# Performance work log

Hardware: AMD Instinct MI355X
Metric: run time of the kernel (lower is better)

## Reference

```python
import jax, jax.numpy as jnp
import numpy as np

N = 8192
EPS = 1e-6


def setup_inputs() -> dict:
    key = jax.random.key(0)
    k1, k2, k3, k4 = jax.random.split(key, 4)
    P_risk = jax.random.normal(k1, (N,), dtype=jnp.float32)
    P_surv = jax.random.normal(k2, (N,), dtype=jnp.float32)
    T = jax.random.uniform(k3, (N,), dtype=jnp.float32)
    E = jax.random.randint(k4, (N,), 0, 2, dtype=jnp.int32)
    return {"P_risk": P_risk, "P_surv": P_surv, "T": T, "E": E}


def _compute_loss(P, M, E_eff):
    # P: [N] log-hazards, M: [N, N] float mask, E_eff: [N] effective event weights
    P_exp = jnp.exp(P)
    # sum_j M[i, j] * exp(P[j])  -- masked risk-set sum as a matvec
    P_exp_sum = M @ P_exp
    log_ratio = jnp.log(P_exp / (P_exp_sum + EPS))
    return -jnp.sum(log_ratio * E_eff) / jnp.sum(E_eff)


def reference(P_risk, P_surv, T, E):
    Ef = E.astype(jnp.float32)
    # M_risk[i, j] = 1 if T[i] < T[j]
    M_risk = (T[:, None] < T[None, :]).astype(jnp.float32)
    # M_surv[i, j] = 1 if T[i] > T[j] and E[j] == 1
    M_surv = (T[:, None] > T[None, :]).astype(jnp.float32) * Ef[None, :]

    # mode='risk': E * (row of M_risk nonempty)
    E_risk = Ef * (jnp.sum(M_risk, axis=1) > 0).astype(jnp.float32)
    # mode='surv': just (row of M_surv nonempty)
    E_surv = (jnp.sum(M_surv, axis=1) > 0).astype(jnp.float32)

    loss_risk = _compute_loss(P_risk, M_risk, E_risk)
    loss_surv = _compute_loss(P_surv, M_surv, E_surv)
    return (loss_risk, loss_surv)
```

## Files before the change

### kernel.cpp

```cpp
#include <hip/hip_runtime.h>
#include <math.h>

#define NN 8192
#define EPSF 1e-6f
#define R 8
#define GX (NN / R)


__global__ __launch_bounds__(256) void ds_main(
    const float* __restrict__ Pr, const float* __restrict__ Ps,
    const float* __restrict__ T,  const int* __restrict__ E,
    float4* __restrict__ part) {
  const int tid  = threadIdx.x;
  const int row0 = blockIdx.x * R;

  float Ti[R];
#pragma unroll
  for (int r = 0; r < R; ++r) Ti[r] = T[row0 + r];

  float sr[R], ss[R];
#pragma unroll
  for (int r = 0; r < R; ++r) { sr[r] = 0.0f; ss[r] = 0.0f; }

  for (int k = 0; k < NN; k += 1024) {
    const int j = k + tid * 4;
    float4 t4  = *(const float4*)(T  + j);
    float4 pr4 = *(const float4*)(Pr + j);
    float4 ps4 = *(const float4*)(Ps + j);
    int4   e4  = *(const int4*)(E  + j);
    float er0 = __expf(pr4.x), er1 = __expf(pr4.y),
          er2 = __expf(pr4.z), er3 = __expf(pr4.w);
    float es0 = e4.x ? __expf(ps4.x) : 0.0f;
    float es1 = e4.y ? __expf(ps4.y) : 0.0f;
    float es2 = e4.z ? __expf(ps4.z) : 0.0f;
    float es3 = e4.w ? __expf(ps4.w) : 0.0f;
#pragma unroll
    for (int r = 0; r < R; ++r) {
      bool g0 = t4.x > Ti[r];  sr[r] += g0 ? er0 : 0.0f;  ss[r] += g0 ? 0.0f : es0;
      bool g1 = t4.y > Ti[r];  sr[r] += g1 ? er1 : 0.0f;  ss[r] += g1 ? 0.0f : es1;
      bool g2 = t4.z > Ti[r];  sr[r] += g2 ? er2 : 0.0f;  ss[r] += g2 ? 0.0f : es2;
      bool g3 = t4.w > Ti[r];  sr[r] += g3 ? er3 : 0.0f;  ss[r] += g3 ? 0.0f : es3;
    }
  }

#pragma unroll
  for (int r = 0; r < R; ++r) {
    for (int off = 32; off > 0; off >>= 1) {
      sr[r] += __shfl_down(sr[r], off);
      ss[r] += __shfl_down(ss[r], off);
    }
  }
  __shared__ float sh[4][2 * R];
  const int wid = tid >> 6, lane = tid & 63;
  if (lane == 0) {
#pragma unroll
    for (int r = 0; r < R; ++r) { sh[wid][r] = sr[r]; sh[wid][R + r] = ss[r]; }
  }
  __syncthreads();
  __shared__ float fin[2 * R];
  if (tid < 2 * R)
    fin[tid] = sh[0][tid] + sh[1][tid] + sh[2][tid] + sh[3][tid];
  __syncthreads();

  float nr = 0.0f, dr = 0.0f, ns = 0.0f, nds = 0.0f;
  if (tid < R) {
    const int   row = row0 + tid;
    const int   e   = E[row];
    const float prv = Pr[row], psv = Ps[row];
    const float es_diag = e ? __expf(psv) : 0.0f;
    const float srv = fin[tid];
    const float ssv = fin[R + tid] - es_diag;
    const float wr = (e != 0 && srv > 0.0f) ? 1.0f : 0.0f;
    const float wsv = (ssv > 0.0f) ? 1.0f : 0.0f;
    nr  = wr  * (prv - logf(srv + EPSF));
    dr  = wr;
    ns  = wsv * (psv - logf(ssv + EPSF));
    nds = wsv;
  }
  if (tid < 64) {
#pragma unroll
    for (int off = R / 2; off > 0; off >>= 1) {
      nr  += __shfl_down(nr,  off);
      dr  += __shfl_down(dr,  off);
      ns  += __shfl_down(ns,  off);
      nds += __shfl_down(nds, off);
    }
    if (tid == 0) part[blockIdx.x] = make_float4(nr, dr, ns, nds);
  }
}

__global__ __launch_bounds__(256) void ds_finalize(
    const float4* __restrict__ part, float* __restrict__ out) {
  float nr = 0.0f, dr = 0.0f, ns = 0.0f, nds = 0.0f;
  for (int i = threadIdx.x; i < GX; i += 256) {
    float4 p = part[i];
    nr += p.x; dr += p.y; ns += p.z; nds += p.w;
  }
  for (int off = 32; off > 0; off >>= 1) {
    nr  += __shfl_down(nr,  off);
    dr  += __shfl_down(dr,  off);
    ns  += __shfl_down(ns,  off);
    nds += __shfl_down(nds, off);
  }
  __shared__ float sh[4][4];
  const int wid = threadIdx.x >> 6, lane = threadIdx.x & 63;
  if (lane == 0) {
    sh[0][wid] = nr; sh[1][wid] = dr; sh[2][wid] = ns; sh[3][wid] = nds;
  }
  __syncthreads();
  if (threadIdx.x == 0) {
    float NR = sh[0][0] + sh[0][1] + sh[0][2] + sh[0][3];
    float DR = sh[1][0] + sh[1][1] + sh[1][2] + sh[1][3];
    float NS = sh[2][0] + sh[2][1] + sh[2][2] + sh[2][3];
    float DS = sh[3][0] + sh[3][1] + sh[3][2] + sh[3][3];
    out[0] = -NR / DR;
    out[1] = -NS / DS;
  }
}

extern "C" void kernel_launch(void* const* d_in, const int* in_sizes, int n_in,
                              void* d_out, int out_size, void* d_ws, size_t ws_size,
                              hipStream_t stream) {
  const float* Pr = (const float*)d_in[0];
  const float* Ps = (const float*)d_in[1];
  const float* T  = (const float*)d_in[2];
  const int*   E  = (const int*)d_in[3];
  float* out = (float*)d_out;

  float4* part = (float4*)d_ws;

  ds_main<<<GX, 256, 0, stream>>>(Pr, Ps, T, E, part);
  ds_finalize<<<1, 256, 0, stream>>>(part, out);
}
```

Measured before the change: 72.99 us.

## Replace quadratic masked risk sums with bucketed counting sort and prefix scans

Drops the O(N^2) pairwise comparison. Elements are bucketed by T into 4096 shared-memory buckets. Prefix and suffix scans of the exp-weighted sums then give the cross-bucket contributions, and only elements inside the same bucket are compared directly after a counting-sort scatter into workspace. Everything now runs in one 1024-thread block, so the finalize launch is gone. The cost is a single-block, serialized, atomic-heavy design whose in-bucket work grows if T values cluster.

```diff
diff --git a/kernel.cpp b/kernel.cpp
--- a/kernel.cpp
+++ b/kernel.cpp
@@ -3,116 +3,152 @@
 
 #define NN 8192
 #define EPSF 1e-6f
-#define R 8
-#define GX (NN / R)
+#define KB_ 4096
+#define NT 1024
+#define EPT (NN / NT)
+#define BPT (KB_ / NT)
 
 
-__global__ __launch_bounds__(256) void ds_main(
+__device__ __forceinline__ int bucket_of(float t) {
+  int b = (int)(t * (float)KB_);
+  b = b < 0 ? 0 : b;
+  return b > (KB_ - 1) ? (KB_ - 1) : b;
+}
+
+__device__ __forceinline__ void scan_excl(float* a, bool rev,
+                                          float* wTot, float* wBase) {
+  const int t = threadIdx.x, lane = t & 63, wid = t >> 6;
+  float v[BPT]; int phys[BPT];
+#pragma unroll
+  for (int i = 0; i < BPT; ++i) {
+    int p = t * BPT + i;
+    phys[i] = rev ? (KB_ - 1 - p) : p;
+    v[i] = a[phys[i]];
+  }
+  float s = 0.0f;
+#pragma unroll
+  for (int i = 0; i < BPT; ++i) s += v[i];
+  float incl = s;
+#pragma unroll
+  for (int off = 1; off < 64; off <<= 1) {
+    float n = __shfl_up(incl, off);
+    if (lane >= off) incl += n;
+  }
+  if (lane == 63) wTot[wid] = incl;
+  __syncthreads();
+  if (t < 16) {
+    float w = wTot[t], wi = w;
+#pragma unroll
+    for (int off = 1; off < 16; off <<= 1) {
+      float n = __shfl_up(wi, off);
+      if (t >= off) wi += n;
+    }
+    wBase[t] = wi - w;
+  }
+  __syncthreads();
+  float run = wBase[wid] + (incl - s);
+#pragma unroll
+  for (int i = 0; i < BPT; ++i) { a[phys[i]] = run; run += v[i]; }
+  __syncthreads();
+}
+
+__global__ __launch_bounds__(NT) void ds_all(
     const float* __restrict__ Pr, const float* __restrict__ Ps,
     const float* __restrict__ T,  const int* __restrict__ E,
-    float4* __restrict__ part) {
-  const int tid  = threadIdx.x;
-  const int row0 = blockIdx.x * R;
+    float* __restrict__ ws, float* __restrict__ out) {
+  __shared__ float sCnt[KB_];
+  __shared__ float sEr[KB_];
+  __shared__ float sEs[KB_];
+  __shared__ float wTot[16], wBase[16];
+  __shared__ float red[16][4];
 
-  float Ti[R];
+  const int t = threadIdx.x, lane = t & 63, wid = t >> 6;
+  float* serT  = ws;
+  float* serEr = ws + NN;
+  float* serEs = ws + 2 * NN;
+
 #pragma unroll
-  for (int r = 0; r < R; ++r) Ti[r] = T[row0 + r];
+  for (int i = 0; i < BPT; ++i) {
+    sCnt[t * BPT + i] = 0.0f;
+    sEr [t * BPT + i] = 0.0f;
+    sEs [t * BPT + i] = 0.0f;
+  }
+  __syncthreads();
 
-  float sr[R], ss[R];
+  float tv[EPT], prv[EPT], psv[EPT]; int ev[EPT];
 #pragma unroll
-  for (int r = 0; r < R; ++r) { sr[r] = 0.0f; ss[r] = 0.0f; }
+  for (int q = 0; q < EPT; ++q) {
+    const int i = t + NT * q;
+    tv[q] = T[i]; prv[q] = Pr[i]; psv[q] = Ps[i]; ev[q] = E[i];
+  }
+#pragma unroll
+  for (int q = 0; q < EPT; ++q) {
+    const float er = __expf(prv[q]);
+    const float es = ev[q] ? __expf(psv[q]) : 0.0f;
+    const int b = bucket_of(tv[q]);
+    atomicAdd(&sCnt[b], 1.0f);
+    atomicAdd(&sEr[b], er);
+    atomicAdd(&sEs[b], es);
+  }
+  __syncthreads();
 
-  for (int k = 0; k < NN; k += 1024) {
-    const int j = k + tid * 4;
-    float4 t4  = *(const float4*)(T  + j);
-    float4 pr4 = *(const float4*)(Pr + j);
-    float4 ps4 = *(const float4*)(Ps + j);
-    int4   e4  = *(const int4*)(E  + j);
-    float er0 = __expf(pr4.x), er1 = __expf(pr4.y),
-          er2 = __expf(pr4.z), er3 = __expf(pr4.w);
-    float es0 = e4.x ? __expf(ps4.x) : 0.0f;
-    float es1 = e4.y ? __expf(ps4.y) : 0.0f;
-    float es2 = e4.z ? __expf(ps4.z) : 0.0f;
-    float es3 = e4.w ? __expf(ps4.w) : 0.0f;
+  scan_excl(sCnt, false, wTot, wBase);
+  scan_excl(sEr,  true,  wTot, wBase);
+  scan_excl(sEs,  false, wTot, wBase);
+
 #pragma unroll
-    for (int r = 0; r < R; ++r) {
-      bool g0 = t4.x > Ti[r];  sr[r] += g0 ? er0 : 0.0f;  ss[r] += g0 ? 0.0f : es0;
-      bool g1 = t4.y > Ti[r];  sr[r] += g1 ? er1 : 0.0f;  ss[r] += g1 ? 0.0f : es1;
-      bool g2 = t4.z > Ti[r];  sr[r] += g2 ? er2 : 0.0f;  ss[r] += g2 ? 0.0f : es2;
-      bool g3 = t4.w > Ti[r];  sr[r] += g3 ? er3 : 0.0f;  ss[r] += g3 ? 0.0f : es3;
+  for (int q = 0; q < EPT; ++q) {
+    const float er = __expf(prv[q]);
+    const float es = ev[q] ? __expf(psv[q]) : 0.0f;
+    const int b = bucket_of(tv[q]);
+    const int pos = (int)atomicAdd(&sCnt[b], 1.0f);
+    serT [pos] = tv[q];
+    serEr[pos] = er;
+    serEs[pos] = es;
+  }
+  __syncthreads();
+
+  float nr = 0.0f, dr = 0.0f, ns = 0.0f, nds = 0.0f;
+#pragma unroll
+  for (int q = 0; q < EPT; ++q) {
+    const float Ti = tv[q];
+    const int b = bucket_of(Ti);
+    const int start = b ? (int)sCnt[b - 1] : 0;
+    const int end   = (int)sCnt[b];
+    float sr  = sEr[b];
+    float ssi = sEs[b];
+    for (int p = start; p < end; ++p) {
+      const float st = serT[p];
+      sr  += (st >  Ti) ? serEr[p] : 0.0f;
+      ssi += (st <= Ti) ? serEs[p] : 0.0f;
     }
+    const float es_diag = ev[q] ? __expf(psv[q]) : 0.0f;
+    const float ss = ssi - es_diag;
+    const float wr  = (ev[q] != 0 && sr > 0.0f) ? 1.0f : 0.0f;
+    const float wsv = (ss > 0.0f) ? 1.0f : 0.0f;
+    nr  += wr  * (prv[q] - logf(sr + EPSF));
+    dr  += wr;
+    ns  += wsv * (psv[q] - logf(ss + EPSF));
+    nds += wsv;
   }
 
 #pragma unroll
-  for (int r = 0; r < R; ++r) {
-    for (int off = 32; off > 0; off >>= 1) {
-      sr[r] += __shfl_down(sr[r], off);
-      ss[r] += __shfl_down(ss[r], off);
-    }
-  }
-  __shared__ float sh[4][2 * R];
-  const int wid = tid >> 6, lane = tid & 63;
-  if (lane == 0) {
-#pragma unroll
-    for (int r = 0; r < R; ++r) { sh[wid][r] = sr[r]; sh[wid][R + r] = ss[r]; }
-  }
-  __syncthreads();
-  __shared__ float fin[2 * R];
-  if (tid < 2 * R)
-    fin[tid] = sh[0][tid] + sh[1][tid] + sh[2][tid] + sh[3][tid];
-  __syncthreads();
-
-  float nr = 0.0f, dr = 0.0f, ns = 0.0f, nds = 0.0f;
-  if (tid < R) {
-    const int   row = row0 + tid;
-    const int   e   = E[row];
-    const float prv = Pr[row], psv = Ps[row];
-    const float es_diag = e ? __expf(psv) : 0.0f;
-    const float srv = fin[tid];
-    const float ssv = fin[R + tid] - es_diag;
-    const float wr = (e != 0 && srv > 0.0f) ? 1.0f : 0.0f;
-    const float wsv = (ssv > 0.0f) ? 1.0f : 0.0f;
-    nr  = wr  * (prv - logf(srv + EPSF));
-    dr  = wr;
-    ns  = wsv * (psv - logf(ssv + EPSF));
-    nds = wsv;
-  }
-  if (tid < 64) {
-#pragma unroll
-    for (int off = R / 2; off > 0; off >>= 1) {
-      nr  += __shfl_down(nr,  off);
-      dr  += __shfl_down(dr,  off);
-      ns  += __shfl_down(ns,  off);
-      nds += __shfl_down(nds, off);
-    }
-    if (tid == 0) part[blockIdx.x] = make_float4(nr, dr, ns, nds);
-  }
-}
-
-__global__ __launch_bounds__(256) void ds_finalize(
-    const float4* __restrict__ part, float* __restrict__ out) {
-  float nr = 0.0f, dr = 0.0f, ns = 0.0f, nds = 0.0f;
-  for (int i = threadIdx.x; i < GX; i += 256) {
-    float4 p = part[i];
-    nr += p.x; dr += p.y; ns += p.z; nds += p.w;
-  }
   for (int off = 32; off > 0; off >>= 1) {
     nr  += __shfl_down(nr,  off);
     dr  += __shfl_down(dr,  off);
     ns  += __shfl_down(ns,  off);
     nds += __shfl_down(nds, off);
   }
-  __shared__ float sh[4][4];
-  const int wid = threadIdx.x >> 6, lane = threadIdx.x & 63;
   if (lane == 0) {
-    sh[0][wid] = nr; sh[1][wid] = dr; sh[2][wid] = ns; sh[3][wid] = nds;
+    red[wid][0] = nr; red[wid][1] = dr; red[wid][2] = ns; red[wid][3] = nds;
   }
   __syncthreads();
-  if (threadIdx.x == 0) {
-    float NR = sh[0][0] + sh[0][1] + sh[0][2] + sh[0][3];
-    float DR = sh[1][0] + sh[1][1] + sh[1][2] + sh[1][3];
-    float NS = sh[2][0] + sh[2][1] + sh[2][2] + sh[2][3];
-    float DS = sh[3][0] + sh[3][1] + sh[3][2] + sh[3][3];
+  if (t == 0) {
+    float NR = 0.0f, DR = 0.0f, NS = 0.0f, DS = 0.0f;
+#pragma unroll
+    for (int w = 0; w < 16; ++w) {
+      NR += red[w][0]; DR += red[w][1]; NS += red[w][2]; DS += red[w][3];
+    }
     out[0] = -NR / DR;
     out[1] = -NS / DS;
   }
@@ -125,10 +161,5 @@
   const float* Ps = (const float*)d_in[1];
   const float* T  = (const float*)d_in[2];
   const int*   E  = (const int*)d_in[3];
-  float* out = (float*)d_out;
-
-  float4* part = (float4*)d_ws;
-
-  ds_main<<<GX, 256, 0, stream>>>(Pr, Ps, T, E, part);
-  ds_finalize<<<1, 256, 0, stream>>>(part, out);
+  ds_all<<<1, NT, 0, stream>>>(Pr, Ps, T, E, (float*)d_ws, (float*)d_out);
 }
```

New measurement: 125.4 us. +71.8%, slower.

## Double rows per block, prefetch next column chunk, and split accumulators

Applied to the files above, without the earlier changes.

Each block now handles 16 rows instead of 8, so the exp of each column element is reused across more rows and half as many blocks recompute it. Loads for the next 1024-column chunk are issued before the current chunk is processed, hiding global memory latency. Each row's sums are split into two partial accumulators to shorten the serial add chains. In exchange, register pressure roughly doubles and the grid shrinks to 512 blocks, which may reduce occupancy.

```diff
diff --git a/kernel.cpp b/kernel.cpp
--- a/kernel.cpp
+++ b/kernel.cpp
@@ -3,11 +3,12 @@
 
 #define NN 8192
 #define EPSF 1e-6f
-#define R 8
+#define R 16
 #define GX (NN / R)
+#define TB 256
 
 
-__global__ __launch_bounds__(256) void ds_main(
+__global__ __launch_bounds__(TB) void ds_main(
     const float* __restrict__ Pr, const float* __restrict__ Ps,
     const float* __restrict__ T,  const int* __restrict__ E,
     float4* __restrict__ part) {
@@ -18,43 +19,70 @@
 #pragma unroll
   for (int r = 0; r < R; ++r) Ti[r] = T[row0 + r];
 
-  float sr[R], ss[R];
+  float2 sr[R], ss[R];
 #pragma unroll
-  for (int r = 0; r < R; ++r) { sr[r] = 0.0f; ss[r] = 0.0f; }
+  for (int r = 0; r < R; ++r) {
+    sr[r] = make_float2(0.0f, 0.0f);
+    ss[r] = make_float2(0.0f, 0.0f);
+  }
+
+  int j0 = tid * 4;
+  float4 t4  = *(const float4*)(T  + j0);
+  float4 pr4 = *(const float4*)(Pr + j0);
+  float4 ps4 = *(const float4*)(Ps + j0);
+  int4   e4  = *(const int4*)(E  + j0);
 
   for (int k = 0; k < NN; k += 1024) {
-    const int j = k + tid * 4;
-    float4 t4  = *(const float4*)(T  + j);
-    float4 pr4 = *(const float4*)(Pr + j);
-    float4 ps4 = *(const float4*)(Ps + j);
-    int4   e4  = *(const int4*)(E  + j);
-    float er0 = __expf(pr4.x), er1 = __expf(pr4.y),
-          er2 = __expf(pr4.z), er3 = __expf(pr4.w);
-    float es0 = e4.x ? __expf(ps4.x) : 0.0f;
-    float es1 = e4.y ? __expf(ps4.y) : 0.0f;
-    float es2 = e4.z ? __expf(ps4.z) : 0.0f;
-    float es3 = e4.w ? __expf(ps4.w) : 0.0f;
+    float4 t4n, pr4n, ps4n; int4 e4n;
+    const bool more = (k + 1024) < NN;
+    if (more) {
+      const int jn = k + 1024 + tid * 4;
+      t4n  = *(const float4*)(T  + jn);
+      pr4n = *(const float4*)(Pr + jn);
+      ps4n = *(const float4*)(Ps + jn);
+      e4n  = *(const int4*)(E  + jn);
+    }
+
+    const float er0 = __expf(pr4.x), er1 = __expf(pr4.y),
+                er2 = __expf(pr4.z), er3 = __expf(pr4.w);
+    const float es0 = e4.x ? __expf(ps4.x) : 0.0f;
+    const float es1 = e4.y ? __expf(ps4.y) : 0.0f;
+    const float es2 = e4.z ? __expf(ps4.z) : 0.0f;
+    const float es3 = e4.w ? __expf(ps4.w) : 0.0f;
+
 #pragma unroll
     for (int r = 0; r < R; ++r) {
-      bool g0 = t4.x > Ti[r];  sr[r] += g0 ? er0 : 0.0f;  ss[r] += g0 ? 0.0f : es0;
-      bool g1 = t4.y > Ti[r];  sr[r] += g1 ? er1 : 0.0f;  ss[r] += g1 ? 0.0f : es1;
-      bool g2 = t4.z > Ti[r];  sr[r] += g2 ? er2 : 0.0f;  ss[r] += g2 ? 0.0f : es2;
-      bool g3 = t4.w > Ti[r];  sr[r] += g3 ? er3 : 0.0f;  ss[r] += g3 ? 0.0f : es3;
+      const float tr = Ti[r];
+      const bool g0 = t4.x > tr, g1 = t4.y > tr,
+                 g2 = t4.z > tr, g3 = t4.w > tr;
+      sr[r].x += g0 ? er0 : 0.0f;
+      sr[r].y += g1 ? er1 : 0.0f;
+      sr[r].x += g2 ? er2 : 0.0f;
+      sr[r].y += g3 ? er3 : 0.0f;
+      ss[r].x += g0 ? 0.0f : es0;
+      ss[r].y += g1 ? 0.0f : es1;
+      ss[r].x += g2 ? 0.0f : es2;
+      ss[r].y += g3 ? 0.0f : es3;
     }
+
+    if (more) { t4 = t4n; pr4 = pr4n; ps4 = ps4n; e4 = e4n; }
   }
 
+  float srf[R], ssf[R];
 #pragma unroll
   for (int r = 0; r < R; ++r) {
+    srf[r] = sr[r].x + sr[r].y;
+    ssf[r] = ss[r].x + ss[r].y;
     for (int off = 32; off > 0; off >>= 1) {
-      sr[r] += __shfl_down(sr[r], off);
-      ss[r] += __shfl_down(ss[r], off);
+      srf[r] += __shfl_down(srf[r], off);
+      ssf[r] += __shfl_down(ssf[r], off);
     }
   }
   __shared__ float sh[4][2 * R];
   const int wid = tid >> 6, lane = tid & 63;
   if (lane == 0) {
 #pragma unroll
-    for (int r = 0; r < R; ++r) { sh[wid][r] = sr[r]; sh[wid][R + r] = ss[r]; }
+    for (int r = 0; r < R; ++r) { sh[wid][r] = srf[r]; sh[wid][R + r] = ssf[r]; }
   }
   __syncthreads();
   __shared__ float fin[2 * R];
@@ -70,7 +98,7 @@
     const float es_diag = e ? __expf(psv) : 0.0f;
     const float srv = fin[tid];
     const float ssv = fin[R + tid] - es_diag;
-    const float wr = (e != 0 && srv > 0.0f) ? 1.0f : 0.0f;
+    const float wr  = (e != 0 && srv > 0.0f) ? 1.0f : 0.0f;
     const float wsv = (ssv > 0.0f) ? 1.0f : 0.0f;
     nr  = wr  * (prv - logf(srv + EPSF));
     dr  = wr;
@@ -129,6 +157,6 @@
 
   float4* part = (float4*)d_ws;
 
-  ds_main<<<GX, 256, 0, stream>>>(Pr, Ps, T, E, part);
+  ds_main<<<GX, TB, 0, stream>>>(Pr, Ps, T, E, part);
   ds_finalize<<<1, 256, 0, stream>>>(part, out);
 }
```

Result: no change. 73.94 us (+1.3%).
